# Kernel optimization log

Measured on AMD Instinct MI355X. Metric: run time of the kernel, lower is better.

The kernel has to match this reference:

```python
import jax, jax.numpy as jnp
import numpy as np
import math

HIDDEN = 2048
HEADS = 16
HEAD_DIM = HIDDEN // HEADS
RANK = HIDDEN // 2  # rank_ratio=0.5
B, S = 1, 4096


def setup_inputs() -> dict:
    key = jax.random.key(0)
    ks = jax.random.split(key, 10)
    sd = lambda fan_in: 1.0 / math.sqrt(fan_in)
    inp = {
        "hidden_states": jax.random.normal(ks[0], (B, S, HIDDEN), dtype=jnp.float32),
        "attention_mask": jnp.zeros((B, 1, S, S), dtype=jnp.float32),
        # low-rank projection weights; Linear weight shape is [out, in]
        "q_V": jax.random.uniform(ks[1], (RANK, HIDDEN), jnp.float32, -sd(HIDDEN), sd(HIDDEN)),
        "q_U": jax.random.uniform(ks[2], (HIDDEN, RANK), jnp.float32, -sd(RANK), sd(RANK)),
        "k_V": jax.random.uniform(ks[3], (RANK, HIDDEN), jnp.float32, -sd(HIDDEN), sd(HIDDEN)),
        "k_U": jax.random.uniform(ks[4], (HIDDEN, RANK), jnp.float32, -sd(RANK), sd(RANK)),
        "v_V": jax.random.uniform(ks[5], (RANK, HIDDEN), jnp.float32, -sd(HIDDEN), sd(HIDDEN)),
        "v_U": jax.random.uniform(ks[6], (HIDDEN, RANK), jnp.float32, -sd(RANK), sd(RANK)),
        "o_W": jax.random.uniform(ks[7], (HIDDEN, HIDDEN), jnp.float32, -sd(HIDDEN), sd(HIDDEN)),
        "o_b": jax.random.uniform(ks[8], (HIDDEN,), jnp.float32, -sd(HIDDEN), sd(HIDDEN)),
    }
    return inp


def _split_heads(x):
    # [B,S,HIDDEN] -> [B,H,S,Dh]
    b, s, _ = x.shape
    return x.reshape(b, s, HEADS, HEAD_DIM).transpose(0, 2, 1, 3)


def reference(hidden_states, attention_mask, q_V, q_U, k_V, k_U, v_V, v_U, o_W, o_b):
    # low-rank QKV: x @ V^T @ U^T
    q = _split_heads((hidden_states @ q_V.T) @ q_U.T)
    k = _split_heads((hidden_states @ k_V.T) @ k_U.T)
    v = _split_heads((hidden_states @ v_V.T) @ v_U.T)
    scores = jnp.einsum("bhqd,bhkd->bhqk", q, k) / math.sqrt(HEAD_DIM)
    scores = scores + attention_mask
    attn = jax.nn.softmax(scores, axis=-1)
    out = jnp.einsum("bhqk,bhkd->bhqd", attn, v)
    out = out.transpose(0, 2, 1, 3).reshape(hidden_states.shape[0], hidden_states.shape[1], HIDDEN)
    out = out @ o_W.T + o_b
    return out
```

## Files before the change

### kernel.cpp

```cpp
#include <hip/hip_runtime.h>

#define HIDDEN 2048
#define HEADS 16
#define HD 128
#define RANK 1024
#define SEQ 4096

typedef __bf16 bf16_t;
typedef __bf16 bf16x8 __attribute__((ext_vector_type(8)));
typedef __bf16 bf16x4 __attribute__((ext_vector_type(4)));
typedef float f32x4 __attribute__((ext_vector_type(4)));

#define MFMA_BF16(a, b, c) __builtin_amdgcn_mfma_f32_16x16x32_bf16((a), (b), (c), 0, 0, 0)

__device__ __forceinline__ void gload16(const bf16_t* g, bf16_t* l) {
  __builtin_amdgcn_global_load_lds(
      (const __attribute__((address_space(1))) unsigned int*)g,
      (__attribute__((address_space(3))) unsigned int*)l, 16, 0, 0);
}

struct CastSeg { const float* s; bf16_t* d; int n4; };
struct CastArgs { CastSeg seg[8]; };

__global__ __launch_bounds__(256) void cast_bf16_kernel(CastArgs a) {
  const int stride = gridDim.x * blockDim.x;
  const int tid0 = blockIdx.x * blockDim.x + threadIdx.x;
#pragma unroll
  for (int i = 0; i < 8; i++) {
    const float4* src = (const float4*)a.seg[i].s;
    bf16x4* dst = (bf16x4*)a.seg[i].d;
    const int n4 = a.seg[i].n4;
    for (int j = tid0; j < n4; j += stride) {
      float4 v = src[j];
      dst[j] = bf16x4{(bf16_t)v.x, (bf16_t)v.y, (bf16_t)v.z, (bf16_t)v.w};
    }
  }
}

__global__ __launch_bounds__(256) void transpose_kernel(const bf16_t* __restrict__ src,
                                                        bf16_t* __restrict__ dst) {
  __shared__ bf16_t Ls[64][68];
  const int s0 = blockIdx.x * 64, c0 = blockIdx.y * 64;
  const int t = threadIdx.x;
  const int r = t >> 3, c8 = t & 7;
#pragma unroll
  for (int p = 0; p < 2; p++) {
    int row = r + p * 32;
    *reinterpret_cast<bf16x8*>(&Ls[row][c8 * 8]) =
        *reinterpret_cast<const bf16x8*>(src + (size_t)(s0 + row) * HIDDEN + c0 + c8 * 8);
  }
  __syncthreads();
#pragma unroll
  for (int p = 0; p < 2; p++) {
    int crow = r + p * 32;
    bf16x8 v;
#pragma unroll
    for (int j = 0; j < 8; j++) v[j] = Ls[c8 * 8 + j][crow];
    *reinterpret_cast<bf16x8*>(dst + (size_t)(c0 + crow) * SEQ + s0 + c8 * 8) = v;
  }
}

template <bool OUT_F32>
__global__ __launch_bounds__(256) void gemm3(const bf16_t* __restrict__ A, int lda, int aOff,
                                             const bf16_t* __restrict__ W0,
                                             const bf16_t* __restrict__ W1,
                                             const bf16_t* __restrict__ W2,
                                             int nPerThird, int K,
                                             void* __restrict__ Cp, int ldc, size_t cOff,
                                             const float* __restrict__ bias, float s0) {
  __shared__ bf16_t As[128 * 32];
  __shared__ bf16_t Bs[128 * 32];
  const int tid = threadIdx.x, lane = tid & 63, wave = tid >> 6;
  const int wr = wave >> 1, wc = wave & 1, quad = lane >> 4, l15 = lane & 15;
  const int n0g = blockIdx.x * 128;
  const int third = n0g / nPerThird;
  const int n0 = n0g - third * nPerThird;
  const bf16_t* W = third == 0 ? W0 : (third == 1 ? W1 : W2);
  const bf16_t* Ab = A + (size_t)third * aOff;
  const int m0 = blockIdx.y * 128;
  const float sc = (third == 0) ? s0 : 1.f;

  f32x4 acc[4][4];
#pragma unroll
  for (int i = 0; i < 4; i++)
#pragma unroll
    for (int j = 0; j < 4; j++) acc[i][j] = f32x4{0.f, 0.f, 0.f, 0.f};

  const int KT = K >> 5;
  for (int kt = 0; kt < KT; ++kt) {
#pragma unroll
    for (int i = 0; i < 2; i++) {
      int slot = (wave * 2 + i) * 64 + lane;
      int row = slot >> 2, cp = slot & 3;
      int cl = cp ^ ((row >> 1) & 3);
      gload16(Ab + (size_t)(m0 + row) * lda + kt * 32 + cl * 8, As + (size_t)(wave * 2 + i) * 512);
    }
#pragma unroll
    for (int i = 0; i < 2; i++) {
      int slot = (wave * 2 + i) * 64 + lane;
      int row = slot >> 2, cp = slot & 3;
      int cl = cp ^ ((row >> 1) & 3);
      gload16(W + (size_t)(n0 + row) * K + kt * 32 + cl * 8, Bs + (size_t)(wave * 2 + i) * 512);
    }
    __syncthreads();

    bf16x8 af[4], bfr[4];
#pragma unroll
    for (int mt = 0; mt < 4; mt++) {
      int row = wr * 64 + mt * 16 + l15;
      int phys = quad ^ ((row >> 1) & 3);
      af[mt] = *reinterpret_cast<const bf16x8*>(As + row * 32 + phys * 8);
    }
#pragma unroll
    for (int nt = 0; nt < 4; nt++) {
      int row = wc * 64 + nt * 16 + l15;
      int phys = quad ^ ((row >> 1) & 3);
      bfr[nt] = *reinterpret_cast<const bf16x8*>(Bs + row * 32 + phys * 8);
    }
#pragma unroll
    for (int mt = 0; mt < 4; mt++)
#pragma unroll
      for (int nt = 0; nt < 4; nt++) acc[mt][nt] = MFMA_BF16(af[mt], bfr[nt], acc[mt][nt]);
    __syncthreads();
  }

#pragma unroll
  for (int nt = 0; nt < 4; nt++) {
    int col = n0 + wc * 64 + nt * 16 + l15;
    float bv = 0.f;
    if constexpr (OUT_F32) bv = bias[col];
#pragma unroll
    for (int mt = 0; mt < 4; mt++) {
      int rowb = m0 + wr * 64 + mt * 16 + quad * 4;
#pragma unroll
      for (int r = 0; r < 4; r++) {
        float vx = acc[mt][nt][r];
        if constexpr (OUT_F32)
          ((float*)Cp + (size_t)third * cOff)[(size_t)(rowb + r) * ldc + col] = vx + bv;
        else
          ((bf16_t*)Cp + (size_t)third * cOff)[(size_t)(rowb + r) * ldc + col] = (bf16_t)(vx * sc);
      }
    }
  }
}

__global__ __launch_bounds__(256, 2) void attn_kernel(const bf16_t* __restrict__ qb,
                                                      const bf16_t* __restrict__ kb,
                                                      const bf16_t* __restrict__ vtp,
                                                      const float* __restrict__ mask,
                                                      bf16_t* __restrict__ ao) {
  __shared__ bf16_t Ks[2][64 * 128];
  __shared__ bf16_t Vs[2][128 * 64];
  const int tid = threadIdx.x, lane = tid & 63, w = tid >> 6;
  const int quad = lane >> 4, l15 = lane & 15;
  const int head = blockIdx.x, q0 = blockIdx.y * 128;
  const float LOG2E = 1.4426950408889634f;

  bf16x8 qf[2][4];
#pragma unroll
  for (int qt = 0; qt < 2; qt++)
#pragma unroll
    for (int ks = 0; ks < 4; ks++)
      qf[qt][ks] = *reinterpret_cast<const bf16x8*>(
          qb + (size_t)(q0 + w * 32 + qt * 16 + l15) * HIDDEN + head * HD + ks * 32 + quad * 8);

  f32x4 O[8][2];
#pragma unroll
  for (int dt = 0; dt < 8; dt++)
#pragma unroll
    for (int qt = 0; qt < 2; qt++) O[dt][qt] = f32x4{0.f, 0.f, 0.f, 0.f};
  float lacc[2] = {0.f, 0.f};

  auto stageKV = [&](int kt, int buf) {
    const int sk0 = kt * 64;
#pragma unroll
    for (int i = 0; i < 4; i++) {
      int slot = (w * 4 + i) * 64 + lane;
      int row = slot >> 4, cp = slot & 15;
      int cl = cp ^ ((row & 3) | ((row & 8) >> 1));
      gload16(kb + (size_t)(sk0 + row) * HIDDEN + head * HD + cl * 8,
              &Ks[buf][(size_t)(w * 4 + i) * 512]);
    }
#pragma unroll
    for (int i = 0; i < 4; i++) {
      int slot = (w * 4 + i) * 64 + lane;
      int row = slot >> 3, cp = slot & 7;
      int cl = cp ^ (row & 7);
      gload16(vtp + (size_t)(head * HD + row) * SEQ + sk0 + cl * 8,
              &Vs[buf][(size_t)(w * 4 + i) * 512]);
    }
  };

  stageKV(0, 0);

  const int sK = (l15 & 3) | (((l15 >> 2) & 1) << 2);
  const int rA0 = ((l15 >> 2) << 3) + (l15 & 3);

  for (int kt = 0; kt < SEQ / 64; ++kt) {
    const int sk0 = kt * 64;
    const int buf = kt & 1;
    __syncthreads();
    stageKV(kt + 1, buf ^ 1);

    f32x4 mv[2][2][2];
#pragma unroll
    for (int kp = 0; kp < 2; kp++)
#pragma unroll
      for (int sub = 0; sub < 2; sub++)
#pragma unroll
        for (int qt = 0; qt < 2; qt++)
          mv[kp][sub][qt] = *reinterpret_cast<const f32x4*>(
              mask + (size_t)(q0 + w * 32 + qt * 16 + l15) * SEQ + sk0 + kp * 32 + quad * 8 +
              sub * 4);

    f32x4 sacc[2][2][2];
#pragma unroll
    for (int kp = 0; kp < 2; kp++)
#pragma unroll
      for (int sub = 0; sub < 2; sub++)
#pragma unroll
        for (int qt = 0; qt < 2; qt++) sacc[kp][sub][qt] = f32x4{0.f, 0.f, 0.f, 0.f};
#pragma unroll
    for (int ks = 0; ks < 4; ks++) {
      int phys = (ks * 4 + quad) ^ sK;
#pragma unroll
      for (int kp = 0; kp < 2; kp++)
#pragma unroll
        for (int sub = 0; sub < 2; sub++) {
          int rowA = kp * 32 + sub * 4 + rA0;
          bf16x8 ak = *reinterpret_cast<const bf16x8*>(&Ks[buf][rowA * 128 + phys * 8]);
#pragma unroll
          for (int qt = 0; qt < 2; qt++)
            sacc[kp][sub][qt] = MFMA_BF16(ak, qf[qt][ks], sacc[kp][sub][qt]);
        }
    }

    bf16x8 pf[2][2];
#pragma unroll
    for (int kp = 0; kp < 2; kp++)
#pragma unroll
      for (int sub = 0; sub < 2; sub++)
#pragma unroll
        for (int qt = 0; qt < 2; qt++) {
          f32x4 e;
#pragma unroll
          for (int r = 0; r < 4; r++)
            e[r] = exp2f(sacc[kp][sub][qt][r] + mv[kp][sub][qt][r] * LOG2E);
          lacc[qt] += (e[0] + e[1]) + (e[2] + e[3]);
#pragma unroll
          for (int r = 0; r < 4; r++) pf[kp][qt][sub * 4 + r] = (bf16_t)e[r];
        }

#pragma unroll
    for (int kp = 0; kp < 2; kp++)
#pragma unroll
      for (int dt = 0; dt < 8; dt++) {
        int row = dt * 16 + l15;
        int phys = (kp * 4 + quad) ^ (l15 & 7);
        bf16x8 av = *reinterpret_cast<const bf16x8*>(&Vs[buf][row * 64 + phys * 8]);
#pragma unroll
        for (int qt = 0; qt < 2; qt++) O[dt][qt] = MFMA_BF16(av, pf[kp][qt], O[dt][qt]);
      }
  }

#pragma unroll
  for (int qt = 0; qt < 2; qt++) {
    float l = lacc[qt];
    l += __shfl_xor(l, 16, 64);
    l += __shfl_xor(l, 32, 64);
    lacc[qt] = 1.f / l;
  }
#pragma unroll
  for (int dt = 0; dt < 8; dt++)
#pragma unroll
    for (int qt = 0; qt < 2; qt++) {
      int q = q0 + w * 32 + qt * 16 + l15;
      int d = head * HD + dt * 16 + quad * 4;
      f32x4 o = O[dt][qt];
      bf16x4 ov = {(bf16_t)(o[0] * lacc[qt]), (bf16_t)(o[1] * lacc[qt]),
                   (bf16_t)(o[2] * lacc[qt]), (bf16_t)(o[3] * lacc[qt])};
      *reinterpret_cast<bf16x4*>(ao + (size_t)q * HIDDEN + d) = ov;
    }
}

extern "C" void kernel_launch(void* const* d_in, const int* in_sizes, int n_in,
                              void* d_out, int out_size, void* d_ws, size_t ws_size,
                              hipStream_t stream) {
  (void)in_sizes; (void)n_in; (void)out_size; (void)ws_size;
  const float* x = (const float*)d_in[0];
  const float* mask = (const float*)d_in[1];
  const float* qV = (const float*)d_in[2];
  const float* qU = (const float*)d_in[3];
  const float* kV = (const float*)d_in[4];
  const float* kU = (const float*)d_in[5];
  const float* vV = (const float*)d_in[6];
  const float* vU = (const float*)d_in[7];
  const float* oW = (const float*)d_in[8];
  const float* ob = (const float*)d_in[9];
  float* out = (float*)d_out;

  char* ws = (char*)d_ws;
  const size_t MB = 1ull << 20;
  bf16_t* xb  = (bf16_t*)(ws);
  bf16_t* tmp = (bf16_t*)(ws + 16 * MB);
  bf16_t* qkv = (bf16_t*)(ws + 40 * MB);
  bf16_t* qVb = (bf16_t*)(ws + 88 * MB);
  bf16_t* qUb = (bf16_t*)(ws + 92 * MB);
  bf16_t* kVb = (bf16_t*)(ws + 96 * MB);
  bf16_t* kUb = (bf16_t*)(ws + 100 * MB);
  bf16_t* vVb = (bf16_t*)(ws + 104 * MB);
  bf16_t* vUb = (bf16_t*)(ws + 108 * MB);
  bf16_t* oWb = (bf16_t*)(ws + 112 * MB);

  const float kQScale = 0.088388347648318447f * 1.4426950408889634f;

  CastArgs ca;
  ca.seg[0] = {x, xb, SEQ * HIDDEN / 4};
  ca.seg[1] = {qV, qVb, RANK * HIDDEN / 4};
  ca.seg[2] = {qU, qUb, HIDDEN * RANK / 4};
  ca.seg[3] = {kV, kVb, RANK * HIDDEN / 4};
  ca.seg[4] = {kU, kUb, HIDDEN * RANK / 4};
  ca.seg[5] = {vV, vVb, RANK * HIDDEN / 4};
  ca.seg[6] = {vU, vUb, HIDDEN * RANK / 4};
  ca.seg[7] = {oW, oWb, HIDDEN * HIDDEN / 4};
  cast_bf16_kernel<<<2048, 256, 0, stream>>>(ca);

  gemm3<false><<<dim3(24, 32), 256, 0, stream>>>(xb, HIDDEN, 0, qVb, kVb, vVb, RANK, HIDDEN,
                                                 tmp, 3 * RANK, (size_t)RANK, nullptr, 1.f);
  gemm3<false><<<dim3(48, 32), 256, 0, stream>>>(tmp, 3 * RANK, RANK, qUb, kUb, vUb, HIDDEN, RANK,
                                                 qkv, HIDDEN, (size_t)SEQ * HIDDEN, nullptr,
                                                 kQScale);
  transpose_kernel<<<dim3(SEQ / 64, HIDDEN / 64), 256, 0, stream>>>(qkv + 2 * (size_t)SEQ * HIDDEN, tmp);
  attn_kernel<<<dim3(HEADS, SEQ / 128), 256, 0, stream>>>(qkv, qkv + (size_t)SEQ * HIDDEN, tmp, mask, xb);
  gemm3<true><<<dim3(16, 32), 256, 0, stream>>>(xb, HIDDEN, 0, oWb, oWb, oWb, HIDDEN, HIDDEN,
                                                out, HIDDEN, 0, ob, 1.f);
}
```

Baseline: 596.1 us.

## Fuse V transpose into GEMM epilogue and software-pipeline attention QK/PV stages

The second low-rank GEMM now writes the V third directly in transposed [HIDDEN][SEQ] layout, so the separate transpose kernel and its extra pass over V are gone. The attention loop is restructured so the QK^T for tile t+1 overlaps with the PV for tile t, using triple-buffered V tiles in shared memory and raised wave priority around the MFMA section. This adds LDS usage (an extra V buffer), which may reduce occupancy. The transposed epilogue also writes to memory with a strided pattern (4 contiguous bf16 per column).

```diff
diff --git a/kernel.cpp b/kernel.cpp
--- a/kernel.cpp
+++ b/kernel.cpp
@@ -37,37 +37,15 @@
   }
 }
 
-__global__ __launch_bounds__(256) void transpose_kernel(const bf16_t* __restrict__ src,
-                                                        bf16_t* __restrict__ dst) {
-  __shared__ bf16_t Ls[64][68];
-  const int s0 = blockIdx.x * 64, c0 = blockIdx.y * 64;
-  const int t = threadIdx.x;
-  const int r = t >> 3, c8 = t & 7;
-#pragma unroll
-  for (int p = 0; p < 2; p++) {
-    int row = r + p * 32;
-    *reinterpret_cast<bf16x8*>(&Ls[row][c8 * 8]) =
-        *reinterpret_cast<const bf16x8*>(src + (size_t)(s0 + row) * HIDDEN + c0 + c8 * 8);
-  }
-  __syncthreads();
-#pragma unroll
-  for (int p = 0; p < 2; p++) {
-    int crow = r + p * 32;
-    bf16x8 v;
-#pragma unroll
-    for (int j = 0; j < 8; j++) v[j] = Ls[c8 * 8 + j][crow];
-    *reinterpret_cast<bf16x8*>(dst + (size_t)(c0 + crow) * SEQ + s0 + c8 * 8) = v;
-  }
-}
-
-template <bool OUT_F32>
+template <int OUT_MODE>
 __global__ __launch_bounds__(256) void gemm3(const bf16_t* __restrict__ A, int lda, int aOff,
                                              const bf16_t* __restrict__ W0,
                                              const bf16_t* __restrict__ W1,
                                              const bf16_t* __restrict__ W2,
                                              int nPerThird, int K,
                                              void* __restrict__ Cp, int ldc, size_t cOff,
-                                             const float* __restrict__ bias, float s0) {
+                                             const float* __restrict__ bias, float s0,
+                                             bf16_t* __restrict__ Ct) {
   __shared__ bf16_t As[128 * 32];
   __shared__ bf16_t Bs[128 * 32];
   const int tid = threadIdx.x, lane = tid & 63, wave = tid >> 6;
@@ -124,18 +102,35 @@
     __syncthreads();
   }
 
+  if constexpr (OUT_MODE == 2) {
+    if (third == 2) {
+#pragma unroll
+      for (int nt = 0; nt < 4; nt++) {
+        int col = n0 + wc * 64 + nt * 16 + l15;
+#pragma unroll
+        for (int mt = 0; mt < 4; mt++) {
+          int rowb = m0 + wr * 64 + mt * 16 + quad * 4;
+          bf16x4 tv = {(bf16_t)acc[mt][nt][0], (bf16_t)acc[mt][nt][1],
+                       (bf16_t)acc[mt][nt][2], (bf16_t)acc[mt][nt][3]};
+          *reinterpret_cast<bf16x4*>(Ct + (size_t)col * SEQ + rowb) = tv;
+        }
+      }
+      return;
+    }
+  }
+
 #pragma unroll
   for (int nt = 0; nt < 4; nt++) {
     int col = n0 + wc * 64 + nt * 16 + l15;
     float bv = 0.f;
-    if constexpr (OUT_F32) bv = bias[col];
+    if constexpr (OUT_MODE == 1) bv = bias[col];
 #pragma unroll
     for (int mt = 0; mt < 4; mt++) {
       int rowb = m0 + wr * 64 + mt * 16 + quad * 4;
 #pragma unroll
       for (int r = 0; r < 4; r++) {
         float vx = acc[mt][nt][r];
-        if constexpr (OUT_F32)
+        if constexpr (OUT_MODE == 1)
           ((float*)Cp + (size_t)third * cOff)[(size_t)(rowb + r) * ldc + col] = vx + bv;
         else
           ((bf16_t*)Cp + (size_t)third * cOff)[(size_t)(rowb + r) * ldc + col] = (bf16_t)(vx * sc);
@@ -150,11 +145,12 @@
                                                       const float* __restrict__ mask,
                                                       bf16_t* __restrict__ ao) {
   __shared__ bf16_t Ks[2][64 * 128];
-  __shared__ bf16_t Vs[2][128 * 64];
+  __shared__ bf16_t Vs[3][128 * 64];
   const int tid = threadIdx.x, lane = tid & 63, w = tid >> 6;
   const int quad = lane >> 4, l15 = lane & 15;
   const int head = blockIdx.x, q0 = blockIdx.y * 128;
   const float LOG2E = 1.4426950408889634f;
+  const int NT = SEQ / 64;
 
   bf16x8 qf[2][4];
 #pragma unroll
@@ -171,38 +167,32 @@
     for (int qt = 0; qt < 2; qt++) O[dt][qt] = f32x4{0.f, 0.f, 0.f, 0.f};
   float lacc[2] = {0.f, 0.f};
 
-  auto stageKV = [&](int kt, int buf) {
-    const int sk0 = kt * 64;
+  auto stageK = [&](int kt, int buf) {
 #pragma unroll
     for (int i = 0; i < 4; i++) {
       int slot = (w * 4 + i) * 64 + lane;
       int row = slot >> 4, cp = slot & 15;
       int cl = cp ^ ((row & 3) | ((row & 8) >> 1));
-      gload16(kb + (size_t)(sk0 + row) * HIDDEN + head * HD + cl * 8,
+      gload16(kb + (size_t)(kt * 64 + row) * HIDDEN + head * HD + cl * 8,
               &Ks[buf][(size_t)(w * 4 + i) * 512]);
     }
+  };
+  auto stageV = [&](int kt, int buf) {
 #pragma unroll
     for (int i = 0; i < 4; i++) {
       int slot = (w * 4 + i) * 64 + lane;
       int row = slot >> 3, cp = slot & 7;
       int cl = cp ^ (row & 7);
-      gload16(vtp + (size_t)(head * HD + row) * SEQ + sk0 + cl * 8,
+      gload16(vtp + (size_t)(head * HD + row) * SEQ + kt * 64 + cl * 8,
               &Vs[buf][(size_t)(w * 4 + i) * 512]);
     }
   };
-
-  stageKV(0, 0);
 
   const int sK = (l15 & 3) | (((l15 >> 2) & 1) << 2);
   const int rA0 = ((l15 >> 2) << 3) + (l15 & 3);
 
-  for (int kt = 0; kt < SEQ / 64; ++kt) {
-    const int sk0 = kt * 64;
-    const int buf = kt & 1;
-    __syncthreads();
-    stageKV(kt + 1, buf ^ 1);
-
-    f32x4 mv[2][2][2];
+  f32x4 mv[2][2][2];
+  auto loadMask = [&](int kt) {
 #pragma unroll
     for (int kp = 0; kp < 2; kp++)
 #pragma unroll
@@ -210,10 +200,12 @@
 #pragma unroll
         for (int qt = 0; qt < 2; qt++)
           mv[kp][sub][qt] = *reinterpret_cast<const f32x4*>(
-              mask + (size_t)(q0 + w * 32 + qt * 16 + l15) * SEQ + sk0 + kp * 32 + quad * 8 +
+              mask + (size_t)(q0 + w * 32 + qt * 16 + l15) * SEQ + kt * 64 + kp * 32 + quad * 8 +
               sub * 4);
-
-    f32x4 sacc[2][2][2];
+  };
+
+  f32x4 sacc[2][2][2];
+  auto qkT = [&](int buf) {
 #pragma unroll
     for (int kp = 0; kp < 2; kp++)
 #pragma unroll
@@ -234,8 +226,10 @@
             sacc[kp][sub][qt] = MFMA_BF16(ak, qf[qt][ks], sacc[kp][sub][qt]);
         }
     }
-
-    bf16x8 pf[2][2];
+  };
+
+  bf16x8 pf[2][2];
+  auto softmaxF = [&]() {
 #pragma unroll
     for (int kp = 0; kp < 2; kp++)
 #pragma unroll
@@ -250,18 +244,46 @@
 #pragma unroll
           for (int r = 0; r < 4; r++) pf[kp][qt][sub * 4 + r] = (bf16_t)e[r];
         }
-
+  };
+
+  auto pv = [&](const bf16_t* Vb) {
 #pragma unroll
     for (int kp = 0; kp < 2; kp++)
 #pragma unroll
       for (int dt = 0; dt < 8; dt++) {
         int row = dt * 16 + l15;
         int phys = (kp * 4 + quad) ^ (l15 & 7);
-        bf16x8 av = *reinterpret_cast<const bf16x8*>(&Vs[buf][row * 64 + phys * 8]);
+        bf16x8 av = *reinterpret_cast<const bf16x8*>(&Vb[row * 64 + phys * 8]);
 #pragma unroll
         for (int qt = 0; qt < 2; qt++) O[dt][qt] = MFMA_BF16(av, pf[kp][qt], O[dt][qt]);
       }
-  }
+  };
+
+  stageK(0, 0);
+  stageV(0, 0);
+  stageK(1, 1);
+  stageV(1, 1);
+  loadMask(0);
+  __syncthreads();
+  qkT(0);
+
+  int vb_pv = 0;
+  int vb_st = 2;
+  for (int t = 0; t < NT - 1; ++t) {
+    softmaxF();
+    __syncthreads();
+    stageK(t + 2, t & 1);
+    stageV(t + 2, vb_st);
+    loadMask(t + 1);
+    __builtin_amdgcn_s_setprio(1);
+    qkT((t + 1) & 1);
+    pv(&Vs[vb_pv][0]);
+    __builtin_amdgcn_s_setprio(0);
+    vb_pv = vb_pv == 2 ? 0 : vb_pv + 1;
+    vb_st = vb_st == 2 ? 0 : vb_st + 1;
+  }
+  softmaxF();
+  pv(&Vs[vb_pv][0]);
 
 #pragma unroll
   for (int qt = 0; qt < 2; qt++) {
@@ -311,6 +333,7 @@
   bf16_t* vVb = (bf16_t*)(ws + 104 * MB);
   bf16_t* vUb = (bf16_t*)(ws + 108 * MB);
   bf16_t* oWb = (bf16_t*)(ws + 112 * MB);
+  bf16_t* vt = qkv + 2 * (size_t)SEQ * HIDDEN;
 
   const float kQScale = 0.088388347648318447f * 1.4426950408889634f;
 
@@ -325,13 +348,13 @@
   ca.seg[7] = {oW, oWb, HIDDEN * HIDDEN / 4};
   cast_bf16_kernel<<<2048, 256, 0, stream>>>(ca);
 
-  gemm3<false><<<dim3(24, 32), 256, 0, stream>>>(xb, HIDDEN, 0, qVb, kVb, vVb, RANK, HIDDEN,
-                                                 tmp, 3 * RANK, (size_t)RANK, nullptr, 1.f);
-  gemm3<false><<<dim3(48, 32), 256, 0, stream>>>(tmp, 3 * RANK, RANK, qUb, kUb, vUb, HIDDEN, RANK,
-                                                 qkv, HIDDEN, (size_t)SEQ * HIDDEN, nullptr,
-                                                 kQScale);
-  transpose_kernel<<<dim3(SEQ / 64, HIDDEN / 64), 256, 0, stream>>>(qkv + 2 * (size_t)SEQ * HIDDEN, tmp);
-  attn_kernel<<<dim3(HEADS, SEQ / 128), 256, 0, stream>>>(qkv, qkv + (size_t)SEQ * HIDDEN, tmp, mask, xb);
-  gemm3<true><<<dim3(16, 32), 256, 0, stream>>>(xb, HIDDEN, 0, oWb, oWb, oWb, HIDDEN, HIDDEN,
-                                                out, HIDDEN, 0, ob, 1.f);
-}
+  gemm3<0><<<dim3(24, 32), 256, 0, stream>>>(xb, HIDDEN, 0, qVb, kVb, vVb, RANK, HIDDEN,
+                                             tmp, 3 * RANK, (size_t)RANK, nullptr, 1.f, nullptr);
+  gemm3<2><<<dim3(48, 32), 256, 0, stream>>>(tmp, 3 * RANK, RANK, qUb, kUb, vUb, HIDDEN, RANK,
+                                             qkv, HIDDEN, (size_t)SEQ * HIDDEN, nullptr,
+                                             kQScale, vt);
+  attn_kernel<<<dim3(HEADS, SEQ / 128), 256, 0, stream>>>(qkv, qkv + (size_t)SEQ * HIDDEN, vt,
+                                                          mask, xb);
+  gemm3<1><<<dim3(16, 32), 256, 0, stream>>>(xb, HIDDEN, 0, oWb, oWb, oWb, HIDDEN, HIDDEN,
+                                             out, HIDDEN, 0, ob, 1.f, nullptr);
+}
```

Measured after the change: 584.3 us. -2.0%, faster.
